# Kernel tuning notes

Measured on AMD Instinct MI355X. Metric: run time of the kernel, lower is better.

## Reference

```python
import jax, jax.numpy as jnp
import numpy as np

LOG8 = float(np.log(8.0))


def setup_inputs() -> dict:
    key = jax.random.key(0)
    ks = jax.random.split(key, 5)
    B, T, D = 4, 4096, 1024
    s = 1.0 / float(np.sqrt(D))  # torch default Linear init scale
    return {
        "x": jax.random.normal(ks[0], (B, T, D), dtype=jnp.float32),
        "h": jnp.zeros((B, D), dtype=jnp.float32),
        "W_r": jax.random.uniform(ks[1], (D, D), jnp.float32, -s, s),
        "b_r": jax.random.uniform(ks[2], (D,), jnp.float32, -4.0, -2.0),
        "W_i": jax.random.uniform(ks[3], (D, D), jnp.float32, -s, s),
        "b_i": jnp.zeros((D,), dtype=jnp.float32),
        "W_x": jax.random.uniform(ks[4], (D, D), jnp.float32, -s, s),
    }


def reference(x, h, W_r, b_r, W_i, b_i, W_x):
    # x: (B, T, D); torch Linear is y = x @ W.T + b with W of shape (out, in)
    r = jax.nn.sigmoid(jnp.einsum('btd,ed->bte', x, W_r) + b_r)   # recurrence gate
    i = jax.nn.sigmoid(jnp.einsum('btd,ed->bte', x, W_i) + b_i)   # input gate
    a = jnp.exp(-jax.nn.softplus(LOG8 * r))                        # data-dependent decay in (0,1)
    gate = jnp.sqrt(jnp.clip(1.0 - a * a, 1e-6))
    u = gate * (i * jnp.einsum('btd,ed->bte', x, W_x))             # per-step input term

    # diagonal linear recurrence h_t = a_t * h_{t-1} + u_t, scanned over time
    def step(h_prev, au):
        a_t, u_t = au  # each (B, D)
        h_new = a_t * h_prev + u_t
        return h_new, h_new

    a_t = jnp.swapaxes(a, 0, 1)  # (T, B, D)
    u_t = jnp.swapaxes(u, 0, 1)
    h_last, out = jax.lax.scan(step, h, (a_t, u_t))
    output = jnp.swapaxes(out, 0, 1)  # (B, T, D)
    return output, h_last
```

## Files before the change

### kernel.cpp

```cpp
#include <hip/hip_runtime.h>
#include <stdint.h>

#define D_DIM 1024
#define T_DIM 4096
#define B_DIM 4
#define M_DIM 16384
#define NX 16777216UL
#define NW 1048576UL
#define NTOT 19922944UL
#define LOG8F 2.0794415416798357f
#define CHUNK_L 64
#define NCHUNK 64
#define WARM 16
#define NT 32

typedef __attribute__((ext_vector_type(4))) float f32x4;
typedef __attribute__((ext_vector_type(8))) short bf16x8;

__device__ __forceinline__ unsigned short f2bf(float f) {
    unsigned u = __float_as_uint(f);
    u += 0x7fffu + ((u >> 16) & 1u);
    return (unsigned short)(u >> 16);
}
__device__ __forceinline__ unsigned packbf2(float x, float y) {
    unsigned ux = __float_as_uint(x);
    ux = (ux + 0x7fffu + ((ux >> 16) & 1u)) >> 16;
    unsigned uy = __float_as_uint(y);
    uy = (uy + 0x7fffu + ((uy >> 16) & 1u)) & 0xffff0000u;
    return ux | uy;
}
__device__ __forceinline__ float bfu(unsigned short p) {
    return __uint_as_float((unsigned)p << 16);
}
__device__ __forceinline__ float sigm(float x) { return 1.0f / (1.0f + __expf(-x)); }

__device__ __forceinline__ void gl_lds16(const void* g, void* l) {
    __builtin_amdgcn_global_load_lds(
        (const __attribute__((address_space(1))) void*)g,
        (__attribute__((address_space(3))) void*)l, 16, 0, 0);
}

__global__ __launch_bounds__(256) void cvt_kernel(
    const float* __restrict__ x, const float* __restrict__ Wr,
    const float* __restrict__ Wi, const float* __restrict__ Wx,
    unsigned short* __restrict__ xb, unsigned short* __restrict__ wb)
{
    const size_t stride = (size_t)gridDim.x * 256 * 8;
    for (size_t i = ((size_t)blockIdx.x * 256 + threadIdx.x) * 8;
         i < NTOT; i += stride) {
        const float* src;
        unsigned short* dst;
        size_t off;
        if (i < NX) {
            src = x; dst = xb; off = i;
        } else {
            size_t j = i - NX;
            size_t w = j >> 20;
            off = j & (NW - 1);
            src = (w == 0) ? Wr : (w == 1 ? Wi : Wx);
            dst = wb + w * NW;
        }
        float4 v0 = *(const float4*)(src + off);
        float4 v1 = *(const float4*)(src + off + 4);
        uint4 o;
        o.x = packbf2(v0.x, v0.y);
        o.y = packbf2(v0.z, v0.w);
        o.z = packbf2(v1.x, v1.y);
        o.w = packbf2(v1.z, v1.w);
        *(uint4*)(dst + off) = o;
    }
}

__global__ __launch_bounds__(512, 2) void fused_gemm(
    const unsigned short* __restrict__ xb, const unsigned short* __restrict__ wb,
    const float* __restrict__ b_r, const float* __restrict__ b_i,
    unsigned short* __restrict__ a_out, float* __restrict__ u_out,
    float* __restrict__ wtail)
{
    __shared__ __align__(16) unsigned short lds[4][16384];

    const int tid  = threadIdx.x;
    const int lane = tid & 63;
    const int wave = tid >> 6;
    const int wm = wave & 1;
    const int wn = wave >> 1;
    const int m0 = ((int)blockIdx.x >> 3) * 128;
    const int d0 = ((int)blockIdx.x & 7) * 128;
    const int frow = lane & 15;
    const int kgrp = lane >> 4;

    const int r0 = tid >> 2;
    const int cgs = (tid & 3) ^ ((r0 >> 1) & 3);
    const unsigned short* srcA  = xb + (size_t)(m0 + r0) * D_DIM + cgs * 8;
    const unsigned short* srcB0 = wb + (size_t)(d0 + r0) * D_DIM + cgs * 8;
    const unsigned short* srcB1 = srcB0 + NW;
    const unsigned short* srcB2 = srcB0 + 2 * NW;

    int offA[4], offB[3][2];
    #pragma unroll
    for (int i = 0; i < 4; i++) {
        const int row = wm * 64 + i * 16 + frow;
        offA[i] = row * 32 + ((kgrp ^ ((row >> 1) & 3)) << 3);
    }
    #pragma unroll
    for (int w = 0; w < 3; w++)
        #pragma unroll
        for (int j = 0; j < 2; j++) {
            const int row = wn * 32 + j * 16 + frow;
            offB[w][j] = (1 + w) * 4096 + row * 32 + ((kgrp ^ ((row >> 1) & 3)) << 3);
        }

    f32x4 acc[3][4][2];
    #pragma unroll
    for (int w = 0; w < 3; w++)
        #pragma unroll
        for (int i = 0; i < 4; i++)
            #pragma unroll
            for (int j = 0; j < 2; j++) acc[w][i][j] = (f32x4){0.f, 0.f, 0.f, 0.f};

    auto stage = [&](int t) {
        const int buf = t & 3;
        const int k0 = t << 5;
        gl_lds16(srcA  + k0, &lds[buf][tid * 8]);
        gl_lds16(srcB0 + k0, &lds[buf][4096 + tid * 8]);
        gl_lds16(srcB1 + k0, &lds[buf][8192 + tid * 8]);
        gl_lds16(srcB2 + k0, &lds[buf][12288 + tid * 8]);
    };

    bf16x8 af_a[4], af_b[4], bf_a[3][2], bf_b[3][2];

    stage(0); stage(1); stage(2);
    asm volatile("s_waitcnt vmcnt(8)" ::: "memory");
    __builtin_amdgcn_s_barrier();
    asm volatile("" ::: "memory");
    #pragma unroll
    for (int i = 0; i < 4; i++) af_a[i] = *(const bf16x8*)&lds[0][offA[i]];
    #pragma unroll
    for (int w = 0; w < 3; w++)
        #pragma unroll
        for (int j = 0; j < 2; j++) bf_a[w][j] = *(const bf16x8*)&lds[0][offB[w][j]];

#define STEP(T, AFC, BFC, AFN, BFN, VM)                                       \
    {                                                                         \
        asm volatile("s_waitcnt vmcnt(" #VM ")" ::: "memory");                \
        __builtin_amdgcn_s_barrier();                                         \
        asm volatile("" ::: "memory");                                        \
        if ((T) + 3 < NT) stage((T) + 3);                                     \
        if ((T) + 1 < NT) {                                                   \
            const unsigned short* nb = lds[((T) + 1) & 3];                    \
            _Pragma("unroll")                                                 \
            for (int i = 0; i < 4; i++)                                       \
                AFN[i] = *(const bf16x8*)&nb[offA[i]];                        \
            _Pragma("unroll")                                                 \
            for (int w = 0; w < 3; w++)                                       \
                _Pragma("unroll")                                             \
                for (int j = 0; j < 2; j++)                                   \
                    BFN[w][j] = *(const bf16x8*)&nb[offB[w][j]];              \
        }                                                                     \
        __builtin_amdgcn_s_setprio(1);                                        \
        _Pragma("unroll")                                                     \
        for (int w = 0; w < 3; w++)                                           \
            _Pragma("unroll")                                                 \
            for (int i = 0; i < 4; i++)                                       \
                _Pragma("unroll")                                             \
                for (int j = 0; j < 2; j++)                                   \
                    acc[w][i][j] = __builtin_amdgcn_mfma_f32_16x16x32_bf16(   \
                        AFC[i], BFC[w][j], acc[w][i][j], 0, 0, 0);            \
        __builtin_amdgcn_s_setprio(0);                                        \
    }

    for (int t = 0; t < 28; t += 2) {
        STEP(t,     af_a, bf_a, af_b, bf_b, 4);
        STEP(t + 1, af_b, bf_b, af_a, bf_a, 4);
    }
    STEP(28, af_a, bf_a, af_b, bf_b, 4);
    STEP(29, af_b, bf_b, af_a, bf_a, 4);
    STEP(30, af_a, bf_a, af_b, bf_b, 0);
    STEP(31, af_b, bf_b, af_a, bf_a, 0);
#undef STEP

    const int mb = m0 + wm * 64 + kgrp * 4;
    const int db = d0 + wn * 32 + frow;
    #pragma unroll
    for (int j = 0; j < 2; j++) {
        const int d = db + j * 16;
        const float br = b_r[d];
        const float bi = b_i[d];
        #pragma unroll
        for (int i = 0; i < 4; i++) {
            const int m = mb + i * 16;
            #pragma unroll
            for (int r = 0; r < 4; r++) {
                const int mr = m + r;
                const size_t idx = (size_t)mr * D_DIM + d;
                float rg = sigm(acc[0][i][j][r] + br);
                float a = sigm(-LOG8F * rg);
                a_out[idx] = f2bf(a);
                float g = sqrtf(fmaxf(1.0f - a * a, 1e-6f));
                float uval = g * sigm(acc[1][i][j][r] + bi) * acc[2][i][j][r];
                u_out[idx] = uval;
                if (i == 3) {
                    const int t = mr & 4095;
                    if (t < 4032) {
                        const int b = mr >> 12;
                        const size_t widx =
                            ((((size_t)b << 6) + ((t >> 6) + 1)) * WARM +
                             (t & 15)) * D_DIM + d;
                        wtail[widx] = uval;
                    }
                }
            }
        }
    }
}

__global__ __launch_bounds__(256) void scan_fused(
    const unsigned short* __restrict__ a, const float* __restrict__ wtail,
    const float* __restrict__ h0, float* __restrict__ out)
{
    int tid = blockIdx.x * 256 + threadIdx.x;
    int d = tid & 1023;
    int bc = tid >> 10;
    int b = bc >> 6;
    int c = bc & (NCHUNK - 1);
    float h;
    if (c == 0) {
        h = h0[b * D_DIM + d];
    } else {
        h = 0.0f;
        size_t abase = ((size_t)b * T_DIM + (size_t)c * CHUNK_L - WARM) * D_DIM + d;
        size_t wbase = ((size_t)bc * WARM) * D_DIM + d;
        #pragma unroll 8
        for (int t = 0; t < WARM; t++) {
            float av = bfu(a[abase + (size_t)t * D_DIM]);
            float uv = wtail[wbase + (size_t)t * D_DIM];
            h = av * h + uv;
        }
    }
    size_t base = ((size_t)b * T_DIM + (size_t)c * CHUNK_L) * D_DIM + d;
    #pragma unroll 8
    for (int t = 0; t < CHUNK_L; t++) {
        size_t idx = base + (size_t)t * D_DIM;
        float av = bfu(a[idx]);
        float uv = out[idx];
        h = av * h + uv;
        out[idx] = h;
    }
    if (c == NCHUNK - 1)
        out[(size_t)M_DIM * D_DIM + b * D_DIM + d] = h;
}

extern "C" void kernel_launch(void* const* d_in, const int* in_sizes, int n_in,
                              void* d_out, int out_size, void* d_ws, size_t ws_size,
                              hipStream_t stream)
{
    const float* x  = (const float*)d_in[0];
    const float* h0 = (const float*)d_in[1];
    const float* Wr = (const float*)d_in[2];
    const float* br = (const float*)d_in[3];
    const float* Wi = (const float*)d_in[4];
    const float* bi = (const float*)d_in[5];
    const float* Wx = (const float*)d_in[6];
    float* out = (float*)d_out;

    char* ws = (char*)d_ws;
    unsigned short* xb = (unsigned short*)ws;
    unsigned short* wb = (unsigned short*)(ws + 33554432);
    unsigned short* a_buf = (unsigned short*)(ws + 33554432 + 6291456);
    float* wtail = (float*)(ws + 33554432 + 6291456 + 33554432);

    cvt_kernel<<<2048, 256, 0, stream>>>(x, Wr, Wi, Wx, xb, wb);
    fused_gemm<<<1024, 512, 0, stream>>>(xb, wb, br, bi, a_buf, out, wtail);
    scan_fused<<<1024, 256, 0, stream>>>(a_buf, wtail, h0, out);
}
```

Baseline: 288.0 us.

## Switch GEMM main loop to double-buffered K=64 tiles with 8-way swizzle

```diff
diff --git a/kernel.cpp b/kernel.cpp
--- a/kernel.cpp
+++ b/kernel.cpp
@@ -12,7 +12,7 @@
 #define CHUNK_L 64
 #define NCHUNK 64
 #define WARM 16
-#define NT 32
+#define NT2 16
 
 typedef __attribute__((ext_vector_type(4))) float f32x4;
 typedef __attribute__((ext_vector_type(8))) short bf16x8;
@@ -77,7 +77,7 @@
     unsigned short* __restrict__ a_out, float* __restrict__ u_out,
     float* __restrict__ wtail)
 {
-    __shared__ __align__(16) unsigned short lds[4][16384];
+    __shared__ __align__(16) unsigned short lds[2][32768];
 
     const int tid  = threadIdx.x;
     const int lane = tid & 63;
@@ -89,25 +89,29 @@
     const int frow = lane & 15;
     const int kgrp = lane >> 4;
 
-    const int r0 = tid >> 2;
-    const int cgs = (tid & 3) ^ ((r0 >> 1) & 3);
-    const unsigned short* srcA  = xb + (size_t)(m0 + r0) * D_DIM + cgs * 8;
-    const unsigned short* srcB0 = wb + (size_t)(d0 + r0) * D_DIM + cgs * 8;
-    const unsigned short* srcB1 = srcB0 + NW;
-    const unsigned short* srcB2 = srcB0 + 2 * NW;
-
-    int offA[4], offB[3][2];
+    const int r_0 = tid >> 3;
+    const int c_0 = tid & 7;
+    const int cgs = c_0 ^ (r_0 & 7);
+    const unsigned short* srcA = xb + (size_t)(m0 + r_0) * D_DIM + cgs * 8;
+    const unsigned short* srcB = wb + (size_t)(d0 + r_0) * D_DIM + cgs * 8;
+
+    int offA[4][2], offB[3][2][2];
     #pragma unroll
     for (int i = 0; i < 4; i++) {
         const int row = wm * 64 + i * 16 + frow;
-        offA[i] = row * 32 + ((kgrp ^ ((row >> 1) & 3)) << 3);
+        #pragma unroll
+        for (int ks = 0; ks < 2; ks++)
+            offA[i][ks] = row * 64 + ((((ks * 4) + kgrp) ^ (row & 7)) << 3);
     }
     #pragma unroll
     for (int w = 0; w < 3; w++)
         #pragma unroll
         for (int j = 0; j < 2; j++) {
             const int row = wn * 32 + j * 16 + frow;
-            offB[w][j] = (1 + w) * 4096 + row * 32 + ((kgrp ^ ((row >> 1) & 3)) << 3);
+            #pragma unroll
+            for (int ks = 0; ks < 2; ks++)
+                offB[w][j][ks] = 8192 + w * 8192 + row * 64 +
+                                 ((((ks * 4) + kgrp) ^ (row & 7)) << 3);
         }
 
     f32x4 acc[3][4][2];
@@ -119,65 +123,54 @@
             for (int j = 0; j < 2; j++) acc[w][i][j] = (f32x4){0.f, 0.f, 0.f, 0.f};
 
     auto stage = [&](int t) {
-        const int buf = t & 3;
-        const int k0 = t << 5;
-        gl_lds16(srcA  + k0, &lds[buf][tid * 8]);
-        gl_lds16(srcB0 + k0, &lds[buf][4096 + tid * 8]);
-        gl_lds16(srcB1 + k0, &lds[buf][8192 + tid * 8]);
-        gl_lds16(srcB2 + k0, &lds[buf][12288 + tid * 8]);
+        unsigned short* L = &lds[t & 1][0];
+        const int k0 = t << 6;
+        gl_lds16(srcA + k0,                &L[tid * 8]);
+        gl_lds16(srcA + 64 * D_DIM + k0,   &L[4096 + tid * 8]);
+        #pragma unroll
+        for (int w = 0; w < 3; w++) {
+            const unsigned short* bw = srcB + (size_t)w * NW + k0;
+            gl_lds16(bw,                &L[8192 + w * 8192 + tid * 8]);
+            gl_lds16(bw + 64 * D_DIM,   &L[8192 + w * 8192 + 4096 + tid * 8]);
+        }
     };
 
-    bf16x8 af_a[4], af_b[4], bf_a[3][2], bf_b[3][2];
-
-    stage(0); stage(1); stage(2);
-    asm volatile("s_waitcnt vmcnt(8)" ::: "memory");
-    __builtin_amdgcn_s_barrier();
-    asm volatile("" ::: "memory");
-    #pragma unroll
-    for (int i = 0; i < 4; i++) af_a[i] = *(const bf16x8*)&lds[0][offA[i]];
-    #pragma unroll
-    for (int w = 0; w < 3; w++)
-        #pragma unroll
-        for (int j = 0; j < 2; j++) bf_a[w][j] = *(const bf16x8*)&lds[0][offB[w][j]];
-
-#define STEP(T, AFC, BFC, AFN, BFN, VM)                                       \
-    {                                                                         \
-        asm volatile("s_waitcnt vmcnt(" #VM ")" ::: "memory");                \
-        __builtin_amdgcn_s_barrier();                                         \
-        asm volatile("" ::: "memory");                                        \
-        if ((T) + 3 < NT) stage((T) + 3);                                     \
-        if ((T) + 1 < NT) {                                                   \
-            const unsigned short* nb = lds[((T) + 1) & 3];                    \
-            _Pragma("unroll")                                                 \
-            for (int i = 0; i < 4; i++)                                       \
-                AFN[i] = *(const bf16x8*)&nb[offA[i]];                        \
-            _Pragma("unroll")                                                 \
-            for (int w = 0; w < 3; w++)                                       \
-                _Pragma("unroll")                                             \
-                for (int j = 0; j < 2; j++)                                   \
-                    BFN[w][j] = *(const bf16x8*)&nb[offB[w][j]];              \
-        }                                                                     \
-        __builtin_amdgcn_s_setprio(1);                                        \
-        _Pragma("unroll")                                                     \
-        for (int w = 0; w < 3; w++)                                           \
-            _Pragma("unroll")                                                 \
-            for (int i = 0; i < 4; i++)                                       \
-                _Pragma("unroll")                                             \
-                for (int j = 0; j < 2; j++)                                   \
-                    acc[w][i][j] = __builtin_amdgcn_mfma_f32_16x16x32_bf16(   \
-                        AFC[i], BFC[w][j], acc[w][i][j], 0, 0, 0);            \
-        __builtin_amdgcn_s_setprio(0);                                        \
-    }
-
-    for (int t = 0; t < 28; t += 2) {
-        STEP(t,     af_a, bf_a, af_b, bf_b, 4);
-        STEP(t + 1, af_b, bf_b, af_a, bf_a, 4);
-    }
-    STEP(28, af_a, bf_a, af_b, bf_b, 4);
-    STEP(29, af_b, bf_b, af_a, bf_a, 4);
-    STEP(30, af_a, bf_a, af_b, bf_b, 0);
-    STEP(31, af_b, bf_b, af_a, bf_a, 0);
-#undef STEP
+    stage(0);
+
+    for (int t = 0; t < NT2; ++t) {
+        asm volatile("s_waitcnt vmcnt(0)" ::: "memory");
+        __builtin_amdgcn_s_barrier();
+        asm volatile("" ::: "memory");
+        if (t + 1 < NT2) stage(t + 1);
+
+        const unsigned short* Lb = &lds[t & 1][0];
+        bf16x8 af[4][2], bf[3][2][2];
+        #pragma unroll
+        for (int i = 0; i < 4; i++)
+            #pragma unroll
+            for (int ks = 0; ks < 2; ks++)
+                af[i][ks] = *(const bf16x8*)&Lb[offA[i][ks]];
+        #pragma unroll
+        for (int w = 0; w < 3; w++)
+            #pragma unroll
+            for (int j = 0; j < 2; j++)
+                #pragma unroll
+                for (int ks = 0; ks < 2; ks++)
+                    bf[w][j][ks] = *(const bf16x8*)&Lb[offB[w][j][ks]];
+
+        __builtin_amdgcn_s_setprio(1);
+        #pragma unroll
+        for (int ks = 0; ks < 2; ks++)
+            #pragma unroll
+            for (int w = 0; w < 3; w++)
+                #pragma unroll
+                for (int i = 0; i < 4; i++)
+                    #pragma unroll
+                    for (int j = 0; j < 2; j++)
+                        acc[w][i][j] = __builtin_amdgcn_mfma_f32_16x16x32_bf16(
+                            af[i][ks], bf[w][j][ks], acc[w][i][j], 0, 0, 0);
+        __builtin_amdgcn_s_setprio(0);
+    }
 
     const int mb = m0 + wm * 64 + kgrp * 4;
     const int db = d0 + wn * 32 + frow;
```

Measured after the change: 292.9 us. No clear change (+1.7%).
